# Kernel optimization log

Measured on AMD Instinct MI355X. Metric: run time of the kernel, lower is better.

Reference implementation:

```python
import jax, jax.numpy as jnp
import numpy as np

DIM = 199  # number of graph nodes, hardcoded in the source repo
K_HOP = 3


def _khop_support(n, k):
    # Ring graph adjacency with self loops, then k-hop reachability mask.
    A = np.eye(n, dtype=np.float64)
    idx = np.arange(n)
    A[idx, (idx + 1) % n] = 1.0
    A[(idx + 1) % n, idx] = 1.0
    S = np.linalg.matrix_power(A, k)
    return (S > 0).astype(np.float32)


def setup_inputs() -> dict:
    key = jax.random.key(0)
    kx, kk = jax.random.split(key)
    batch, n, f = 256, DIM, 1024
    x = jax.random.normal(kx, (batch, n, f), dtype=jnp.float32)
    support = jnp.asarray(_khop_support(n, K_HOP))
    # glorot-uniform-ish kernel
    limit = float(np.sqrt(6.0 / (n + n)))
    kernel = jax.random.uniform(kk, (n, n), minval=-limit, maxval=limit, dtype=jnp.float32)
    bias = jnp.zeros((f,), dtype=jnp.float32)
    return {"x": x, "support": support, "kernel": kernel, "bias": bias}


def reference(x, support, kernel, bias):
    # W = k-hop mask * trainable kernel  -> masked dense matmul over nodes
    W = support * kernel  # [N, N]
    # out[b,m,f] = sum_n x[b,n,f] * W[n,m]  (permute-dot-permute in the original)
    out = jnp.einsum('bnf,nm->bmf', x, W)
    out = out + bias  # broadcast over feature dim
    return out  # activation=None -> linear
```

## Files before the change

### kernel.cpp

```cpp
#include <hip/hip_runtime.h>
#include <stdint.h>


__global__ void build_csc_kernel(const float* __restrict__ support,
                                 const float* __restrict__ kern,
                                 int* __restrict__ cnt,
                                 int* __restrict__ idx,
                                 float* __restrict__ val,
                                 int n) {
    const int m = blockIdx.x;
    const int lane = threadIdx.x;
    int base = 0;
    for (int n0 = 0; n0 < n; n0 += 64) {
        const int row = n0 + lane;
        float w = 0.0f;
        if (row < n) w = support[(size_t)row * n + m] * kern[(size_t)row * n + m];
        const unsigned long long mask = __ballot(w != 0.0f);
        const int pos = base + (int)__popcll(mask & ((1ull << lane) - 1ull));
        if (w != 0.0f) {
            idx[(size_t)m * n + pos] = row;
            val[(size_t)m * n + pos] = w;
        }
        base += (int)__popcll(mask);
    }
    if (lane == 0) cnt[m] = base;
}

__global__ __launch_bounds__(256) void spmm_kernel(
    const float4* __restrict__ x, const float* __restrict__ bias,
    const int* __restrict__ cnt, const int* __restrict__ idx,
    const float* __restrict__ val, float4* __restrict__ out,
    int n, int f4, int swizzle) {
    const int blk = blockIdx.x;
    int b, m;
    if (swizzle) {
        const int xcd = blk & 7;
        const int ii = blk >> 3;
        b = xcd + 8 * (ii / n);
        m = ii % n;
    } else {
        b = blk / n;
        m = blk % n;
    }
    const int c = cnt[m];
    const int* __restrict__ ip = idx + (size_t)m * n;
    const float* __restrict__ vp = val + (size_t)m * n;
    const float4* __restrict__ b4 = (const float4*)bias;
    const size_t xbase = (size_t)b * n * f4;
    const size_t obase = ((size_t)b * n + m) * f4;
    for (int t = threadIdx.x; t < f4; t += 256) {
        float4 acc = b4[t];
        for (int j = 0; j < c; ++j) {
            const int nn = ip[j];
            const float w = vp[j];
            const float4 v = x[xbase + (size_t)nn * f4 + t];
            acc.x = fmaf(w, v.x, acc.x);
            acc.y = fmaf(w, v.y, acc.y);
            acc.z = fmaf(w, v.z, acc.z);
            acc.w = fmaf(w, v.w, acc.w);
        }
        out[obase + t] = acc;
    }
}

__global__ __launch_bounds__(256) void dense_fallback_kernel(
    const float4* __restrict__ x, const float* __restrict__ support,
    const float* __restrict__ kern, const float* __restrict__ bias,
    float4* __restrict__ out, int n, int f4) {
    const int blk = blockIdx.x;
    const int b = blk / n;
    const int m = blk % n;
    const float4* __restrict__ b4 = (const float4*)bias;
    const size_t xbase = (size_t)b * n * f4;
    const size_t obase = ((size_t)b * n + m) * f4;
    for (int t = threadIdx.x; t < f4; t += 256) {
        float4 acc = b4[t];
        for (int nn = 0; nn < n; ++nn) {
            const float w = support[(size_t)nn * n + m] * kern[(size_t)nn * n + m];
            if (w != 0.0f) {
                const float4 v = x[xbase + (size_t)nn * f4 + t];
                acc.x = fmaf(w, v.x, acc.x);
                acc.y = fmaf(w, v.y, acc.y);
                acc.z = fmaf(w, v.z, acc.z);
                acc.w = fmaf(w, v.w, acc.w);
            }
        }
        out[obase + t] = acc;
    }
}

extern "C" void kernel_launch(void* const* d_in, const int* in_sizes, int n_in,
                              void* d_out, int out_size, void* d_ws, size_t ws_size,
                              hipStream_t stream) {
    const float* x       = (const float*)d_in[0];
    const float* support = (const float*)d_in[1];
    const float* kern    = (const float*)d_in[2];
    const float* bias    = (const float*)d_in[3];
    float* out = (float*)d_out;

    const int nsq = in_sizes[1];
    int n = 1;
    while (n * n < nsq) ++n;
    const int f = in_sizes[3];
    const int f4 = f / 4;
    const int batch = in_sizes[0] / (n * f);

    const size_t need = ((size_t)n + 2u * (size_t)n * (size_t)n) * 4u;
    if (ws_size >= need && (f % 4) == 0) {
        int* cnt = (int*)d_ws;
        int* idx = cnt + n;
        float* val = (float*)(idx + (size_t)n * n);
        build_csc_kernel<<<n, 64, 0, stream>>>(support, kern, cnt, idx, val, n);
        const int swz = (batch % 8 == 0) ? 1 : 0;
        spmm_kernel<<<batch * n, 256, 0, stream>>>(
            (const float4*)x, bias, cnt, idx, val, (float4*)out, n, f4, swz);
    } else {
        dense_fallback_kernel<<<batch * n, 256, 0, stream>>>(
            (const float4*)x, support, kern, bias, (float4*)out, n, f / 4);
    }
}
```

Before: 371.8 us.

## Process output rows in groups with sliding register window over banded x rows

Each block now computes a contiguous group of output rows (8 groups per batch) instead of one row. When a column's nonzeros form a contiguous 7-wide band, the kernel keeps a sliding window of x rows in registers and loads only one new row per output, so each x row is read about once instead of seven times. Outputs are written with nontemporal stores. The grid shrinks to batch*8 blocks, which lowers parallelism, and the band check depends on the ring/k-hop structure; other columns fall back to the general path.

```diff
diff --git a/kernel.cpp b/kernel.cpp
--- a/kernel.cpp
+++ b/kernel.cpp
@@ -1,6 +1,14 @@
 #include <hip/hip_runtime.h>
 #include <stdint.h>
 
+
+typedef float nt_f4 __attribute__((ext_vector_type(4)));
+
+__device__ __forceinline__ void nt_store4(const float4& a, float4* p) {
+    nt_f4 v;
+    v.x = a.x; v.y = a.y; v.z = a.z; v.w = a.w;
+    __builtin_nontemporal_store(v, (nt_f4*)p);
+}
 
 __global__ void build_csc_kernel(const float* __restrict__ support,
                                  const float* __restrict__ kern,
@@ -26,40 +34,77 @@
     if (lane == 0) cnt[m] = base;
 }
 
-__global__ __launch_bounds__(256) void spmm_kernel(
+__global__ __launch_bounds__(256) void spmm_band_kernel(
     const float4* __restrict__ x, const float* __restrict__ bias,
     const int* __restrict__ cnt, const int* __restrict__ idx,
     const float* __restrict__ val, float4* __restrict__ out,
-    int n, int f4, int swizzle) {
+    int n, int f4, int ngroups, int mg, int swizzle) {
     const int blk = blockIdx.x;
-    int b, m;
+    int b, g;
     if (swizzle) {
         const int xcd = blk & 7;
-        const int ii = blk >> 3;
-        b = xcd + 8 * (ii / n);
-        m = ii % n;
+        const int j = blk >> 3;
+        g = j % ngroups;
+        b = xcd + 8 * (j / ngroups);
     } else {
-        b = blk / n;
-        m = blk % n;
+        b = blk / ngroups;
+        g = blk % ngroups;
     }
-    const int c = cnt[m];
-    const int* __restrict__ ip = idx + (size_t)m * n;
-    const float* __restrict__ vp = val + (size_t)m * n;
+    const int m0 = g * mg;
+    const int m1 = min(n, m0 + mg);
+    const float4* __restrict__ xb = x + (size_t)b * n * f4;
+    float4* __restrict__ ob = out + (size_t)b * n * f4;
     const float4* __restrict__ b4 = (const float4*)bias;
-    const size_t xbase = (size_t)b * n * f4;
-    const size_t obase = ((size_t)b * n + m) * f4;
+
     for (int t = threadIdx.x; t < f4; t += 256) {
-        float4 acc = b4[t];
-        for (int j = 0; j < c; ++j) {
-            const int nn = ip[j];
-            const float w = vp[j];
-            const float4 v = x[xbase + (size_t)nn * f4 + t];
-            acc.x = fmaf(w, v.x, acc.x);
-            acc.y = fmaf(w, v.y, acc.y);
-            acc.z = fmaf(w, v.z, acc.z);
-            acc.w = fmaf(w, v.w, acc.w);
+        const float4 bias4 = b4[t];
+        float4 win[7];
+        float4 nxt;
+        int valid = 0;
+        for (int m = m0; m < m1; ++m) {
+            const int c = cnt[m];
+            const int* __restrict__ ip = idx + (size_t)m * n;
+            const float* __restrict__ vp = val + (size_t)m * n;
+            bool band = (c == 7);
+            if (band) band = (ip[0] == m - 3) && (ip[6] == m + 3);
+            if (band) {
+                if (valid) {
+                    win[0] = win[1]; win[1] = win[2]; win[2] = win[3];
+                    win[3] = win[4]; win[4] = win[5]; win[5] = win[6];
+                    win[6] = nxt;
+                } else {
+#pragma unroll
+                    for (int j = 0; j < 7; ++j)
+                        win[j] = xb[(size_t)(m - 3 + j) * f4 + t];
+                }
+                const int pn = (m + 4 < n) ? (m + 4) : (n - 1);
+                nxt = xb[(size_t)pn * f4 + t];
+                float4 a = bias4;
+#pragma unroll
+                for (int j = 0; j < 7; ++j) {
+                    const float w = vp[j];
+                    a.x = fmaf(w, win[j].x, a.x);
+                    a.y = fmaf(w, win[j].y, a.y);
+                    a.z = fmaf(w, win[j].z, a.z);
+                    a.w = fmaf(w, win[j].w, a.w);
+                }
+                nt_store4(a, &ob[(size_t)m * f4 + t]);
+                valid = 1;
+            } else {
+                float4 a = bias4;
+                for (int j = 0; j < c; ++j) {
+                    const int nn = ip[j];
+                    const float w = vp[j];
+                    const float4 v = xb[(size_t)nn * f4 + t];
+                    a.x = fmaf(w, v.x, a.x);
+                    a.y = fmaf(w, v.y, a.y);
+                    a.z = fmaf(w, v.z, a.z);
+                    a.w = fmaf(w, v.w, a.w);
+                }
+                nt_store4(a, &ob[(size_t)m * f4 + t]);
+                valid = 0;
+            }
         }
-        out[obase + t] = acc;
     }
 }
 
@@ -111,9 +156,12 @@
         int* idx = cnt + n;
         float* val = (float*)(idx + (size_t)n * n);
         build_csc_kernel<<<n, 64, 0, stream>>>(support, kern, cnt, idx, val, n);
+        const int ngroups = 8;
+        const int mg = (n + ngroups - 1) / ngroups;
         const int swz = (batch % 8 == 0) ? 1 : 0;
-        spmm_kernel<<<batch * n, 256, 0, stream>>>(
-            (const float4*)x, bias, cnt, idx, val, (float4*)out, n, f4, swz);
+        spmm_band_kernel<<<batch * ngroups, 256, 0, stream>>>(
+            (const float4*)x, bias, cnt, idx, val, (float4*)out,
+            n, f4, ngroups, mg, swz);
     } else {
         dense_fallback_kernel<<<batch * n, 256, 0, stream>>>(
             (const float4*)x, support, kern, bias, (float4*)out, n, f / 4);
```

Result: slower. 381.1 us (+2.5%).

## Compute four output nodes per block from shared banded x window

Applied to the files above, without the earlier changes.

Adds a band-extraction kernel that stores the 7 diagonal weights per output column and flags columns whose nonzeros all fall inside that band (a fast path). The SpMM kernel now computes 4 consecutive output nodes per block. Each thread loads a 10-row window of x once and reuses it across the 4 outputs, cutting redundant x reads from about 7 per output row to about 2.5. Non-banded or wraparound columns fall back to the CSC gather path. The cost is one extra small launch and more registers per thread for the window.

```diff
diff --git a/kernel.cpp b/kernel.cpp
--- a/kernel.cpp
+++ b/kernel.cpp
@@ -1,6 +1,8 @@
 #include <hip/hip_runtime.h>
 #include <stdint.h>
 
+
+#define CPB 4
 
 __global__ void build_csc_kernel(const float* __restrict__ support,
                                  const float* __restrict__ kern,
@@ -26,40 +28,89 @@
     if (lane == 0) cnt[m] = base;
 }
 
-__global__ __launch_bounds__(256) void spmm_kernel(
+__global__ void build_band_kernel(const float* __restrict__ support,
+                                  const float* __restrict__ kern,
+                                  const int* __restrict__ cnt,
+                                  float* __restrict__ wband,
+                                  int* __restrict__ fastok,
+                                  int n) {
+    const int m = blockIdx.x * blockDim.x + threadIdx.x;
+    if (m >= n) return;
+    int cb = 0;
+    for (int j = 0; j < 7; ++j) {
+        int r = m - 3 + j;
+        if (r < 0) r += n;
+        if (r >= n) r -= n;
+        const float w = support[(size_t)r * n + m] * kern[(size_t)r * n + m];
+        wband[(size_t)m * 8 + j] = w;
+        cb += (w != 0.0f) ? 1 : 0;
+    }
+    wband[(size_t)m * 8 + 7] = 0.0f;
+    fastok[m] = (n >= 7 && cb == cnt[m] && m >= 3 && m <= n - 4) ? 1 : 0;
+}
+
+__global__ __launch_bounds__(256) void spmm_band4_kernel(
     const float4* __restrict__ x, const float* __restrict__ bias,
     const int* __restrict__ cnt, const int* __restrict__ idx,
-    const float* __restrict__ val, float4* __restrict__ out,
-    int n, int f4, int swizzle) {
+    const float* __restrict__ val, const float* __restrict__ wband,
+    const int* __restrict__ fastok, float4* __restrict__ out,
+    int n, int f4, int ngroups, int swizzle) {
     const int blk = blockIdx.x;
-    int b, m;
+    int b, g;
     if (swizzle) {
         const int xcd = blk & 7;
         const int ii = blk >> 3;
-        b = xcd + 8 * (ii / n);
-        m = ii % n;
+        g = ii % ngroups;
+        b = xcd + 8 * (ii / ngroups);
     } else {
-        b = blk / n;
-        m = blk % n;
+        b = blk / ngroups;
+        g = blk % ngroups;
     }
-    const int c = cnt[m];
-    const int* __restrict__ ip = idx + (size_t)m * n;
-    const float* __restrict__ vp = val + (size_t)m * n;
+    const int m0 = g * CPB;
+    const float4* __restrict__ xb = x + (size_t)b * n * f4;
+    float4* __restrict__ ob = out + (size_t)b * n * f4;
     const float4* __restrict__ b4 = (const float4*)bias;
-    const size_t xbase = (size_t)b * n * f4;
-    const size_t obase = ((size_t)b * n + m) * f4;
+
     for (int t = threadIdx.x; t < f4; t += 256) {
-        float4 acc = b4[t];
-        for (int j = 0; j < c; ++j) {
-            const int nn = ip[j];
-            const float w = vp[j];
-            const float4 v = x[xbase + (size_t)nn * f4 + t];
-            acc.x = fmaf(w, v.x, acc.x);
-            acc.y = fmaf(w, v.y, acc.y);
-            acc.z = fmaf(w, v.z, acc.z);
-            acc.w = fmaf(w, v.w, acc.w);
+        const float4 bias4 = b4[t];
+        float4 win[CPB + 6];
+#pragma unroll
+        for (int j = 0; j < CPB + 6; ++j) {
+            int r = m0 - 3 + j;
+            r = (r < 0) ? 0 : ((r >= n) ? (n - 1) : r);
+            win[j] = xb[(size_t)r * f4 + t];
         }
-        out[obase + t] = acc;
+#pragma unroll
+        for (int dm = 0; dm < CPB; ++dm) {
+            const int m = m0 + dm;
+            if (m >= n) break;
+            float4 a = bias4;
+            if (fastok[m]) {
+                const float* __restrict__ wb = wband + (size_t)m * 8;
+#pragma unroll
+                for (int j = 0; j < 7; ++j) {
+                    const float w = wb[j];
+                    a.x = fmaf(w, win[dm + j].x, a.x);
+                    a.y = fmaf(w, win[dm + j].y, a.y);
+                    a.z = fmaf(w, win[dm + j].z, a.z);
+                    a.w = fmaf(w, win[dm + j].w, a.w);
+                }
+            } else {
+                const int c = cnt[m];
+                const int* __restrict__ ip = idx + (size_t)m * n;
+                const float* __restrict__ vp = val + (size_t)m * n;
+                for (int j = 0; j < c; ++j) {
+                    const int nn = ip[j];
+                    const float w = vp[j];
+                    const float4 v = xb[(size_t)nn * f4 + t];
+                    a.x = fmaf(w, v.x, a.x);
+                    a.y = fmaf(w, v.y, a.y);
+                    a.z = fmaf(w, v.z, a.z);
+                    a.w = fmaf(w, v.w, a.w);
+                }
+            }
+            ob[(size_t)m * f4 + t] = a;
+        }
     }
 }
 
@@ -105,15 +156,21 @@
     const int f4 = f / 4;
     const int batch = in_sizes[0] / (n * f);
 
-    const size_t need = ((size_t)n + 2u * (size_t)n * (size_t)n) * 4u;
-    if (ws_size >= need && (f % 4) == 0) {
+    const size_t need = ((size_t)2 * n * n + 10u * (size_t)n) * 4u;
+    if (ws_size >= need && (f % 4) == 0 && n >= 7) {
         int* cnt = (int*)d_ws;
         int* idx = cnt + n;
         float* val = (float*)(idx + (size_t)n * n);
+        float* wband = val + (size_t)n * n;
+        int* fastok = (int*)(wband + (size_t)8 * n);
         build_csc_kernel<<<n, 64, 0, stream>>>(support, kern, cnt, idx, val, n);
+        build_band_kernel<<<(n + 255) / 256, 256, 0, stream>>>(
+            support, kern, cnt, wband, fastok, n);
+        const int ngroups = (n + CPB - 1) / CPB;
         const int swz = (batch % 8 == 0) ? 1 : 0;
-        spmm_kernel<<<batch * n, 256, 0, stream>>>(
-            (const float4*)x, bias, cnt, idx, val, (float4*)out, n, f4, swz);
+        spmm_band4_kernel<<<batch * ngroups, 256, 0, stream>>>(
+            (const float4*)x, bias, cnt, idx, val, wband, fastok,
+            (float4*)out, n, f4, ngroups, swz);
     } else {
         dense_fallback_kernel<<<batch * n, 256, 0, stream>>>(
             (const float4*)x, support, kern, bias, (float4*)out, n, f / 4);
```

Result: faster. 354.5 us (-4.7%).
